# Performance work log

Measured on AMD Instinct MI355X. Metric: run time of the kernel, lower is better.

## Reference

```python
import jax, jax.numpy as jnp
import numpy as np

HEADS = 8
DIM_HEAD = 64
TAU = 0.001        # SoftSort temperature
TEMP = 10.0        # GammaAggregator temperature (EspAttention default temperature=10)
SCALE = DIM_HEAD ** -0.5


def setup_inputs() -> dict:
    key = jax.random.key(0)
    k1, k2, k3, k4 = jax.random.split(key, 4)
    x = jax.random.normal(k1, (4, 128, 512), jnp.float32)
    w_qkv = jax.random.normal(k2, (1536, 512), jnp.float32) * 0.02
    w_out = jax.random.normal(k3, (512, 512), jnp.float32) * 0.02
    b_out = jax.random.normal(k4, (512,), jnp.float32) * 0.02
    return {"x": x, "w_qkv": w_qkv, "w_out": w_out, "b_out": b_out}


def _softsort_p2(scores, tau):
    # scores: [B,H,N,L] -> s: [B,H,L,N]
    s = jnp.swapaxes(scores, -1, -2)
    sorted_s = -jnp.sort(-s, axis=-1)                 # descending sort along N
    # pairwise diff: [B,H,L,N(sorted),N(orig)]
    d = s[..., None, :] - sorted_s[..., :, None]
    return jax.nn.softmax(-(d * d) / tau, axis=-1)    # P_hat [B,H,L,N,N]


def reference(x, w_qkv, w_out, b_out):
    B, N, D = x.shape
    qkv = x @ w_qkv.T                                  # [B,N,3*inner]
    q, k, v = jnp.split(qkv, 3, axis=-1)
    def to_heads(t):
        return jnp.swapaxes(t.reshape(B, N, HEADS, DIM_HEAD), 1, 2)  # [B,H,N,d]
    q, k, v = to_heads(q), to_heads(k), to_heads(v)

    X = q * SCALE
    Y = k * SCALE

    Pu = _softsort_p2(X, TAU)                          # [B,H,L,N,N]
    Pv = _softsort_p2(Y, TAU)                          # [B,H,L,N,N]
    # Gamma = Pu^T @ Pv over the sorted axis
    Gamma = jnp.einsum('bhlki,bhlkj->bhlij', Pu, Pv)   # [B,H,L,N,N]

    # cdist(X, Y, p=2): [B,H,N,N]
    sq = (jnp.sum(X * X, -1)[..., :, None]
          + jnp.sum(Y * Y, -1)[..., None, :]
          - 2.0 * jnp.einsum('bhnd,bhmd->bhnm', X, Y))
    cost = jnp.sqrt(jnp.maximum(sq, 0.0))

    # swds_l = sum_ij cost_ij * Gamma_lij
    swds = jnp.einsum('bhij,bhlij->bhl', cost, Gamma)  # [B,H,L]
    min_s = jnp.min(swds, axis=-1, keepdims=True)
    e = jnp.exp(-TEMP * (swds - min_s))
    weights = e / jnp.sum(e, axis=-1, keepdims=True)   # [B,H,L]

    attn = jnp.einsum('bhl,bhlij->bhij', weights, Gamma)  # [B,H,N,N]

    out = jnp.einsum('bhij,bhjd->bhid', attn, v)       # [B,H,N,d]
    out = jnp.swapaxes(out, 1, 2).reshape(B, N, HEADS * DIM_HEAD)
    out = out @ w_out.T + b_out                        # to_out (dropout=0)
    return out, attn
```

## Files before the change

kernel.cpp:

```cpp
#include <hip/hip_runtime.h>
#include <math.h>

typedef _Float16 f16x8 __attribute__((ext_vector_type(8)));
typedef _Float16 f16x4 __attribute__((ext_vector_type(4)));
typedef float f32x4 __attribute__((ext_vector_type(4)));

#define NSEQ   128
#define DIMH   64
#define NHEAD  8
#define DMODEL 512
#define SCALE  0.125f
#define SPAD   136

#define OFF_X    0
#define OFF_Y    262144
#define OFF_V    524288
#define OFF_COST 786432
#define OFF_SWDS 1310720
#define OFF_W    1312768
#define OFF_OH   1314816
#define OFF_XT   1576960
#define OFF_YT   1839104
#define OFF_ST   2101248
#define OFF_PART 3674112
#define END_PART 12062720

#define PF_SMEM  (NSEQ * SPAD * 2 + (768 + 8) * 4)
#define PH_SMEM  (2 * NSEQ * SPAD * 2 + (128 * 3 + 512 + 8) * 4)

__device__ __forceinline__ f16x8 cvt8(f32x4 a, f32x4 b) {
  f16x8 h;
  h[0] = (_Float16)a[0]; h[1] = (_Float16)a[1]; h[2] = (_Float16)a[2]; h[3] = (_Float16)a[3];
  h[4] = (_Float16)b[0]; h[5] = (_Float16)b[1]; h[6] = (_Float16)b[2]; h[7] = (_Float16)b[3];
  return h;
}

__global__ __launch_bounds__(256) void k_qkv_f(const float* __restrict__ x,
                                               const float* __restrict__ wq,
                                               float* __restrict__ ws) {
  __shared__ _Float16 Ah[64][72];
  __shared__ _Float16 Bh[64][72];
  const int r0 = blockIdx.x * 64, c0 = blockIdx.y * 64;
  const int t = threadIdx.x, w = t >> 6, lane = t & 63;
  const int srow = t >> 2, sk = (t & 3) << 4;
  f32x4 acc[4] = {};
  for (int kc = 0; kc < 512; kc += 64) {
    __syncthreads();
    {
      const float* ap = &x[(size_t)(r0 + srow) * 512 + kc + sk];
      const float* bp = &wq[(size_t)(c0 + srow) * 512 + kc + sk];
      f32x4 a0 = *(const f32x4*)&ap[0], a1 = *(const f32x4*)&ap[4];
      f32x4 a2 = *(const f32x4*)&ap[8], a3 = *(const f32x4*)&ap[12];
      f32x4 b0 = *(const f32x4*)&bp[0], b1 = *(const f32x4*)&bp[4];
      f32x4 b2 = *(const f32x4*)&bp[8], b3 = *(const f32x4*)&bp[12];
      *(f16x8*)&Ah[srow][sk]     = cvt8(a0, a1);
      *(f16x8*)&Ah[srow][sk + 8] = cvt8(a2, a3);
      *(f16x8*)&Bh[srow][sk]     = cvt8(b0, b1);
      *(f16x8*)&Bh[srow][sk + 8] = cvt8(b2, b3);
    }
    __syncthreads();
#pragma unroll
    for (int k0 = 0; k0 < 64; k0 += 32) {
      f16x8 a = *(const f16x8*)&Ah[(w << 4) + (lane & 15)][k0 + ((lane >> 4) << 3)];
#pragma unroll
      for (int fj = 0; fj < 4; ++fj) {
        f16x8 b = *(const f16x8*)&Bh[(fj << 4) + (lane & 15)][k0 + ((lane >> 4) << 3)];
        acc[fj] = __builtin_amdgcn_mfma_f32_16x16x32_f16(a, b, acc[fj], 0, 0, 0);
      }
    }
  }
  float* X = ws + OFF_X; float* Y = ws + OFF_Y; float* V = ws + OFF_V;
  float* XT = ws + OFF_XT; float* YT = ws + OFF_YT;
  const int rowb = r0 + (w << 4) + ((lane >> 4) << 2);
#pragma unroll
  for (int fj = 0; fj < 4; ++fj) {
    const int c = c0 + (fj << 4) + (lane & 15);
    const int which = c >> 9, cc = c & 511, h = cc >> 6, d = cc & 63;
#pragma unroll
    for (int r = 0; r < 4; ++r) {
      const int rr = rowb + r, bb = rr >> 7, n = rr & 127;
      const int bh = bb * NHEAD + h;
      float val = acc[fj][r];
      size_t dst = ((size_t)bh * NSEQ + n) * DIMH + d;
      size_t dstT = ((size_t)bh * DIMH + d) * NSEQ + n;
      if (which == 0)      { X[dst] = val * SCALE; XT[dstT] = val * SCALE; }
      else if (which == 1) { Y[dst] = val * SCALE; YT[dstT] = val * SCALE; }
      else                 V[dst] = val;
    }
  }
}

__global__ __launch_bounds__(256) void k_qkv(const float* __restrict__ x,
                                             const float* __restrict__ wqkv,
                                             float* __restrict__ ws, int wrT) {
  __shared__ float xs[64][65];
  __shared__ float wsm[64][65];
  const int r0 = blockIdx.x * 64;
  const int c0 = blockIdx.y * 64;
  const int t = threadIdx.x;
  const int tr = (t >> 4) << 2;
  const int tc = (t & 15) << 2;
  float acc[4][4] = {};
  for (int k0 = 0; k0 < 512; k0 += 64) {
    for (int idx = t; idx < 64 * 64; idx += 256) {
      int i = idx >> 6, j = idx & 63;
      xs[i][j]  = x[(size_t)(r0 + i) * 512 + k0 + j];
      wsm[i][j] = wqkv[(size_t)(c0 + i) * 512 + k0 + j];
    }
    __syncthreads();
    for (int kk = 0; kk < 64; ++kk) {
      float a[4], b[4];
#pragma unroll
      for (int u = 0; u < 4; ++u) { a[u] = xs[tr + u][kk]; b[u] = wsm[tc + u][kk]; }
#pragma unroll
      for (int u = 0; u < 4; ++u)
#pragma unroll
        for (int w = 0; w < 4; ++w) acc[u][w] += a[u] * b[w];
    }
    __syncthreads();
  }
  float* X = ws + OFF_X; float* Y = ws + OFF_Y; float* V = ws + OFF_V;
  float* XT = ws + OFF_XT; float* YT = ws + OFF_YT;
#pragma unroll
  for (int u = 0; u < 4; ++u) {
    int r = r0 + tr + u; int b = r >> 7, n = r & 127;
#pragma unroll
    for (int w = 0; w < 4; ++w) {
      int c = c0 + tc + w;
      float val = acc[u][w];
      int which = c >> 9;
      int cc = c & 511;
      int h = cc >> 6, d = cc & 63;
      int bh = b * NHEAD + h;
      size_t dst = ((size_t)bh * NSEQ + n) * DIMH + d;
      size_t dstT = ((size_t)bh * DIMH + d) * NSEQ + n;
      if (which == 0)      { X[dst] = val * SCALE; if (wrT) XT[dstT] = val * SCALE; }
      else if (which == 1) { Y[dst] = val * SCALE; if (wrT) YT[dstT] = val * SCALE; }
      else                 V[dst] = val;
    }
  }
}

__global__ __launch_bounds__(256) void k_cost(float* __restrict__ ws) {
  __shared__ float Ys[128 * 64];
  __shared__ float Xs[16 * 64];
  __shared__ float xx[16], yy[128];
  const int bh = blockIdx.x, g = blockIdx.y;
  const int t = threadIdx.x;
  const float* Xg = ws + OFF_X + (size_t)bh * NSEQ * DIMH + (size_t)g * 16 * DIMH;
  const float* Yg = ws + OFF_Y + (size_t)bh * NSEQ * DIMH;
  for (int c = t; c < 1024; c += 256) Xs[c] = Xg[c];
  for (int c = t; c < 8192; c += 256) Ys[c] = Yg[c];
  __syncthreads();
  if (t < 128) {
    float s = 0;
    const f32x4* y4 = (const f32x4*)&Ys[t * 64];
#pragma unroll
    for (int d = 0; d < 16; ++d) { f32x4 v = y4[d]; s += v[0]*v[0]+v[1]*v[1]+v[2]*v[2]+v[3]*v[3]; }
    yy[t] = s;
  } else if (t < 144) {
    int i = t - 128; float s = 0;
    const f32x4* x4 = (const f32x4*)&Xs[i * 64];
#pragma unroll
    for (int d = 0; d < 16; ++d) { f32x4 v = x4[d]; s += v[0]*v[0]+v[1]*v[1]+v[2]*v[2]+v[3]*v[3]; }
    xx[i] = s;
  }
  __syncthreads();
  const int i = t >> 4, j0 = (t & 15) << 3;
  f32x4 xr[16];
#pragma unroll
  for (int d = 0; d < 16; ++d) xr[d] = ((const f32x4*)&Xs[i * 64])[d];
  const float xxi = xx[i];
  float* C = ws + OFF_COST + (size_t)bh * NSEQ * NSEQ + (size_t)(g * 16 + i) * NSEQ + j0;
  f32x4 o0, o1;
#pragma unroll
  for (int jj = 0; jj < 8; ++jj) {
    const f32x4* y4 = (const f32x4*)&Ys[(j0 + jj) * 64];
    float dot = 0;
#pragma unroll
    for (int d = 0; d < 16; ++d) {
      f32x4 xv = xr[d], yv = y4[d];
      dot += xv[0]*yv[0] + xv[1]*yv[1] + xv[2]*yv[2] + xv[3]*yv[3];
    }
    float sq = xxi + yy[j0 + jj] - 2.f * dot;
    float cv = sqrtf(fmaxf(sq, 0.f));
    if (jj < 4) o0[jj] = cv; else o1[jj - 4] = cv;
  }
  *(f32x4*)&C[0] = o0;
  *(f32x4*)&C[4] = o1;
}

__global__ __launch_bounds__(256) void k_sortden(float* __restrict__ ws) {
  __shared__ float s_lds[128], ss_lds[128], den2[256];
  const int bid = blockIdx.x;
  const int t = threadIdx.x;
  const float* src = ws + ((bid & 1) ? OFF_YT : OFF_XT) + (size_t)(bid >> 1) * NSEQ;
  float* st = ws + OFF_ST + (size_t)bid * 384;
  if (t < 128) s_lds[t] = src[t];
  __syncthreads();
  if (t < 128) {
    const float v = s_lds[t];
    int rank = 0;
#pragma unroll 4
    for (int m = 0; m < NSEQ; m += 4) {
      f32x4 u = *(const f32x4*)&s_lds[m];
#pragma unroll
      for (int j = 0; j < 4; ++j)
        rank += (u[j] > v) || (u[j] == v && (m + j) < t);
    }
    ss_lds[rank] = v;
  }
  __syncthreads();
  {
    const int k = t & 127, half = t >> 7;
    const float sk = ss_lds[k];
    const float* sb = s_lds + (half << 6);
    float sum = 0.f;
#pragma unroll 4
    for (int m = 0; m < 64; m += 4) {
      f32x4 u = *(const f32x4*)&sb[m];
#pragma unroll
      for (int j = 0; j < 4; ++j) {
        float d = u[j] - sk;
        sum += __expf(-1000.f * d * d);
      }
    }
    den2[(half << 7) + k] = sum;
  }
  __syncthreads();
  if (t < 128) {
    st[t]       = s_lds[t];
    st[128 + t] = ss_lds[t];
    st[256 + t] = 1.f / (den2[t] + den2[128 + t]);
  }
}

__device__ __forceinline__ void gen_PT(const float* __restrict__ st,
                                       _Float16* __restrict__ PT, int t) {
  const int i = t >> 2, k0 = (t & 3) << 5;
  const float si = st[i];
  const float* ssp = st + 128 + k0;
  const float* ivp = st + 256 + k0;
#pragma unroll
  for (int kb = 0; kb < 32; kb += 8) {
    f32x4 sv0 = *(const f32x4*)&ssp[kb];
    f32x4 sv1 = *(const f32x4*)&ssp[kb + 4];
    f32x4 iv0 = *(const f32x4*)&ivp[kb];
    f32x4 iv1 = *(const f32x4*)&ivp[kb + 4];
    f16x8 pk;
#pragma unroll
    for (int j = 0; j < 4; ++j) {
      float d0 = si - sv0[j];
      float d1 = si - sv1[j];
      pk[j]     = (_Float16)(__expf(-1000.f * d0 * d0) * iv0[j]);
      pk[j + 4] = (_Float16)(__expf(-1000.f * d1 * d1) * iv1[j]);
    }
    *reinterpret_cast<f16x8*>(&PT[i * SPAD + k0 + kb]) = pk;
  }
}

__device__ __forceinline__ f16x8 gen_Afrag(float si, const float* __restrict__ ss,
                                           const float* __restrict__ iv, int k) {
  f32x4 s0 = *(const f32x4*)&ss[k], s1 = *(const f32x4*)&ss[k + 4];
  f32x4 i0 = *(const f32x4*)&iv[k], i1 = *(const f32x4*)&iv[k + 4];
  f16x8 a;
#pragma unroll
  for (int j = 0; j < 4; ++j) {
    float d0 = si - s0[j];
    float d1 = si - s1[j];
    a[j]     = (_Float16)(__expf(-1000.f * d0 * d0) * i0[j]);
    a[j + 4] = (_Float16)(__expf(-1000.f * d1 * d1) * i1[j]);
  }
  return a;
}

__device__ void build_PT(const float* __restrict__ col, _Float16* __restrict__ PT,
                         float* s_, float* ss_, float* inv_, float* den4, int t) {
  if (t < NSEQ) s_[t] = col[(size_t)t * DIMH];
  __syncthreads();
  if (t < NSEQ) {
    const float v = s_[t];
    int rank = 0;
#pragma unroll 4
    for (int m = 0; m < NSEQ; m += 4) {
      f32x4 u = *(const f32x4*)&s_[m];
#pragma unroll
      for (int j = 0; j < 4; ++j)
        rank += (u[j] > v) || (u[j] == v && (m + j) < t);
    }
    ss_[rank] = v;
  }
  __syncthreads();
  {
    const int k = t & 127, q = t >> 7;
    const float sk = ss_[k];
    const float* sb = s_ + (q << 5);
    float sum = 0.f;
#pragma unroll 4
    for (int m = 0; m < 32; m += 4) {
      f32x4 u = *(const f32x4*)&sb[m];
#pragma unroll
      for (int j = 0; j < 4; ++j) {
        float d = u[j] - sk;
        sum += __expf(-1000.f * d * d);
      }
    }
    den4[(q << 7) + k] = sum;
  }
  __syncthreads();
  if (t < NSEQ)
    inv_[t] = 1.f / (den4[t] + den4[128 + t] + den4[256 + t] + den4[384 + t]);
  __syncthreads();
  {
    const int i = t >> 2, k0 = (t & 3) << 5;
    const float si = s_[i];
#pragma unroll
    for (int kb = 0; kb < 32; kb += 8) {
      f32x4 sv0 = *(const f32x4*)&ss_[k0 + kb];
      f32x4 sv1 = *(const f32x4*)&ss_[k0 + kb + 4];
      f32x4 iv0 = *(const f32x4*)&inv_[k0 + kb];
      f32x4 iv1 = *(const f32x4*)&inv_[k0 + kb + 4];
      f16x8 pk;
#pragma unroll
      for (int j = 0; j < 4; ++j) {
        float d0 = si - sv0[j];
        float d1 = si - sv1[j];
        pk[j]     = (_Float16)(__expf(-1000.f * d0 * d0) * iv0[j]);
        pk[j + 4] = (_Float16)(__expf(-1000.f * d1 * d1) * iv1[j]);
      }
      *reinterpret_cast<f16x8*>(&PT[i * SPAD + k0 + kb]) = pk;
    }
  }
  __syncthreads();
}

__device__ __forceinline__ f16x8 fragPT(const _Float16* PT, int baserow, int k0, int lane) {
  return *reinterpret_cast<const f16x8*>(
      &PT[(baserow + (lane & 15)) * SPAD + k0 + ((lane >> 4) << 3)]);
}

__global__ __launch_bounds__(512, 4) void k_pf(float* __restrict__ ws) {
  extern __shared__ char smem[];
  _Float16* PvT = (_Float16*)smem;
  float* aux = (float*)(PvT + NSEQ * SPAD);
  float* red = aux + 768;
  const int blk = blockIdx.x, bh = blk >> 4, lc = blk & 15;
  const int t = threadIdx.x, w = t >> 6, lane = t & 63;
  const int r0 = w << 4;
  const int kq = (lane >> 4) << 3;
  const float* C = ws + OFF_COST + (size_t)bh * NSEQ * NSEQ;
  const int cr = r0 + ((lane >> 4) << 2), cc = lane & 15;
  f32x4 att[8];
#pragma unroll
  for (int b = 0; b < 8; ++b) att[b] = 0;
  float m_run = 3.0e38f, Z = 0.f;
  for (int q = 0; q < 4; ++q) {
    const int l = (lc << 2) + q;
    if (q) __syncthreads();
    const float* stg = ws + OFF_ST + (size_t)(bh * 64 + l) * 768;
    for (int i = t; i < 768; i += 512) aux[i] = stg[i];
    __syncthreads();
    gen_PT(aux + 384, PvT, t);
    __syncthreads();
    const float si = aux[r0 + (lane & 15)];
    const float* ssu = aux + 128;
    const float* ivu = aux + 256;
    f32x4 acc[8];
#pragma unroll
    for (int b = 0; b < 8; ++b) acc[b] = 0;
#pragma unroll
    for (int kc = 0; kc < 4; ++kc) {
      const int k0 = kc << 5;
      f16x8 a = gen_Afrag(si, ssu, ivu, k0 + kq);
#pragma unroll
      for (int fj = 0; fj < 8; ++fj) {
        f16x8 b = fragPT(PvT, fj << 4, k0, lane);
        acc[fj] = __builtin_amdgcn_mfma_f32_16x16x32_f16(a, b, acc[fj], 0, 0, 0);
      }
    }
    float part = 0.f;
#pragma unroll
    for (int fj = 0; fj < 8; ++fj)
#pragma unroll
      for (int r = 0; r < 4; ++r)
        part += acc[fj][r] * C[(cr + r) * NSEQ + (fj << 4) + cc];
#pragma unroll
    for (int off = 32; off >= 1; off >>= 1) part += __shfl_xor(part, off);
    if (lane == 0) red[w] = part;
    __syncthreads();
    float swds = ((red[0] + red[1]) + (red[2] + red[3]))
               + ((red[4] + red[5]) + (red[6] + red[7]));
    if (swds < m_run) {
      float sc = __expf(-10.f * (m_run - swds));
      Z = Z * sc + 1.f;
#pragma unroll
      for (int b = 0; b < 8; ++b) att[b] = att[b] * sc + acc[b];
      m_run = swds;
    } else {
      float e = __expf(-10.f * (swds - m_run));
      Z += e;
#pragma unroll
      for (int b = 0; b < 8; ++b) att[b] += e * acc[b];
    }
  }
  float* P = ws + OFF_PART + (size_t)blk * (NSEQ * NSEQ);
#pragma unroll
  for (int fj = 0; fj < 8; ++fj)
#pragma unroll
    for (int r = 0; r < 4; ++r)
      P[(cr + r) * NSEQ + (fj << 4) + cc] = att[fj][r];
  if (t == 0) {
    ws[OFF_SWDS + blk * 2]     = m_run;
    ws[OFF_SWDS + blk * 2 + 1] = Z;
  }
}

__global__ __launch_bounds__(512, 4) void k_phase1_fb(float* __restrict__ ws) {
  extern __shared__ char smem[];
  _Float16* PuT = (_Float16*)smem;
  _Float16* PvT = PuT + NSEQ * SPAD;
  float* s_   = (float*)(PvT + NSEQ * SPAD);
  float* ss_  = s_ + 128;
  float* inv_ = ss_ + 128;
  float* den4 = inv_ + 128;
  float* red  = den4 + 512;
  const int bhl = blockIdx.x, bh = bhl >> 6, l = bhl & 63;
  const int t = threadIdx.x, w = t >> 6, lane = t & 63;
  build_PT(ws + OFF_X + (size_t)bh * NSEQ * DIMH + l, PuT, s_, ss_, inv_, den4, t);
  build_PT(ws + OFF_Y + (size_t)bh * NSEQ * DIMH + l, PvT, s_, ss_, inv_, den4, t);
  f32x4 acc[8];
#pragma unroll
  for (int b = 0; b < 8; ++b) acc[b] = 0;
  const int r0 = w << 4;
#pragma unroll
  for (int kc = 0; kc < 4; ++kc) {
    const int k0 = kc << 5;
    f16x8 a0 = fragPT(PuT, r0, k0, lane);
#pragma unroll
    for (int fj = 0; fj < 8; ++fj) {
      f16x8 b = fragPT(PvT, fj << 4, k0, lane);
      acc[fj] = __builtin_amdgcn_mfma_f32_16x16x32_f16(a0, b, acc[fj], 0, 0, 0);
    }
  }
  const float* C = ws + OFF_COST + (size_t)bh * NSEQ * NSEQ;
  const int cr = r0 + ((lane >> 4) << 2), cc = lane & 15;
  float part = 0.f;
#pragma unroll
  for (int fj = 0; fj < 8; ++fj)
#pragma unroll
    for (int r = 0; r < 4; ++r)
      part += acc[fj][r] * C[(cr + r) * NSEQ + (fj << 4) + cc];
#pragma unroll
  for (int off = 32; off >= 1; off >>= 1) part += __shfl_xor(part, off);
  if (lane == 0) red[w] = part;
  __syncthreads();
  if (t == 0) {
    float s = 0;
#pragma unroll
    for (int i = 0; i < 8; ++i) s += red[i];
    ws[OFF_SWDS + bhl] = s;
  }
}

__global__ void k_weights(float* __restrict__ ws) {
  const int bh = blockIdx.x;
  const int l = threadIdx.x;
  float v = ws[OFF_SWDS + bh * 64 + l];
  float mn = v;
#pragma unroll
  for (int off = 32; off >= 1; off >>= 1) mn = fminf(mn, __shfl_xor(mn, off));
  float e = __expf(-10.f * (v - mn));
  float sum = e;
#pragma unroll
  for (int off = 32; off >= 1; off >>= 1) sum += __shfl_xor(sum, off);
  ws[OFF_W + bh * 64 + l] = e / sum;
}

__global__ __launch_bounds__(512, 4) void k_phase2_fb(float* __restrict__ ws, float* __restrict__ attn) {
  extern __shared__ char smem[];
  _Float16* PuT = (_Float16*)smem;
  _Float16* PvT = PuT + NSEQ * SPAD;
  float* s_   = (float*)(PvT + NSEQ * SPAD);
  float* ss_  = s_ + 128;
  float* inv_ = ss_ + 128;
  float* den4 = inv_ + 128;
  const int blk = blockIdx.x, bh = blk >> 4, lc = blk & 15;
  const int t = threadIdx.x, w = t >> 6, lane = t & 63;
  const int r0 = w << 4;
  f32x4 att[8];
#pragma unroll
  for (int b = 0; b < 8; ++b) att[b] = 0;
  for (int q = 0; q < 4; ++q) {
    const int l = (lc << 2) + q;
    const float wl = ws[OFF_W + bh * 64 + l];
    build_PT(ws + OFF_X + (size_t)bh * NSEQ * DIMH + l, PuT, s_, ss_, inv_, den4, t);
    build_PT(ws + OFF_Y + (size_t)bh * NSEQ * DIMH + l, PvT, s_, ss_, inv_, den4, t);
    f32x4 acc[8];
#pragma unroll
    for (int b = 0; b < 8; ++b) acc[b] = 0;
#pragma unroll
    for (int kc = 0; kc < 4; ++kc) {
      const int k0 = kc << 5;
      f16x8 a0 = fragPT(PuT, r0, k0, lane);
#pragma unroll
      for (int fj = 0; fj < 8; ++fj) {
        f16x8 b = fragPT(PvT, fj << 4, k0, lane);
        acc[fj] = __builtin_amdgcn_mfma_f32_16x16x32_f16(a0, b, acc[fj], 0, 0, 0);
      }
    }
#pragma unroll
    for (int b = 0; b < 8; ++b) att[b] += wl * acc[b];
  }
  float* A = attn + (size_t)bh * NSEQ * NSEQ;
  const int cr = r0 + ((lane >> 4) << 2), cc = lane & 15;
#pragma unroll
  for (int fj = 0; fj < 8; ++fj)
#pragma unroll
    for (int r = 0; r < 4; ++r)
      atomicAdd(&A[(cr + r) * NSEQ + (fj << 4) + cc], att[fj][r]);
}

__global__ __launch_bounds__(256) void k_avr(float* __restrict__ ws, float* __restrict__ attn) {
  __shared__ float Vs[128 * 64];
  __shared__ float As[16 * 128];
  __shared__ float F[16];
  __shared__ float Zinv_s;
  const int bh = blockIdx.x, g = blockIdx.y;
  const int t = threadIdx.x;
  for (int c = t; c < 8192; c += 256) Vs[c] = ws[OFF_V + (size_t)bh * 8192 + c];
  if (t == 0) {
    float mb[16], zb[16], m = 3.0e38f;
#pragma unroll
    for (int p = 0; p < 16; ++p) {
      mb[p] = ws[OFF_SWDS + (bh * 16 + p) * 2];
      zb[p] = ws[OFF_SWDS + (bh * 16 + p) * 2 + 1];
      m = fminf(m, mb[p]);
    }
    float Zt = 0.f;
#pragma unroll
    for (int p = 0; p < 16; ++p) {
      float f = __expf(-10.f * (mb[p] - m));
      F[p] = f;
      Zt += f * zb[p];
    }
    Zinv_s = 1.f / Zt;
  }
  __syncthreads();
  const float zi = Zinv_s;
  for (int c = t; c < 2048; c += 256) {
    float s = 0.f;
#pragma unroll
    for (int p = 0; p < 16; ++p)
      s += F[p] * ws[OFF_PART + ((size_t)(bh * 16 + p)) * 16384 + (size_t)g * 2048 + c];
    s *= zi;
    As[c] = s;
    attn[(size_t)bh * 16384 + (size_t)g * 2048 + c] = s;
  }
  __syncthreads();
  const int i = t >> 4, dq = t & 15;
  f32x4 acc = {};
  const float* arow = &As[i * 128];
  for (int j = 0; j < 128; ++j) {
    float a = arow[j];
    f32x4 v = ((const f32x4*)&Vs[j * 64])[dq];
    acc += a * v;
  }
  const int b = bh >> 3, h = bh & 7, n = g * 16 + i;
  const size_t obase = ((size_t)(b * NSEQ + n)) * DMODEL + h * DIMH + (dq << 2);
  _Float16* oh16 = (_Float16*)(ws + OFF_XT + 131072) + obase;
  f16x4 hh;
  hh[0] = (_Float16)acc[0]; hh[1] = (_Float16)acc[1];
  hh[2] = (_Float16)acc[2]; hh[3] = (_Float16)acc[3];
  *(f16x4*)oh16 = hh;
}

__global__ __launch_bounds__(256) void k_av(const float* __restrict__ attn, float* __restrict__ ws) {
  __shared__ float Vs[128 * 64];
  __shared__ float As[16 * 128];
  const int bh = blockIdx.x, g = blockIdx.y;
  const int t = threadIdx.x;
  const float* Ag = attn + (size_t)bh * 16384 + (size_t)g * 16 * 128;
  const float* Vg = ws + OFF_V + (size_t)bh * 8192;
  for (int c = t; c < 2048; c += 256) As[c] = Ag[c];
  for (int c = t; c < 8192; c += 256) Vs[c] = Vg[c];
  __syncthreads();
  const int i = t >> 4, dq = t & 15;
  f32x4 acc = {};
  const float* arow = &As[i * 128];
  for (int j = 0; j < 128; ++j) {
    float a = arow[j];
    f32x4 v = ((const f32x4*)&Vs[j * 64])[dq];
    acc += a * v;
  }
  const int b = bh >> 3, h = bh & 7, n = g * 16 + i;
  const size_t obase = ((size_t)(b * NSEQ + n)) * DMODEL + h * DIMH + (dq << 2);
  float* o = ws + OFF_OH + obase;
  *(f32x4*)o = acc;
}

__global__ __launch_bounds__(256) void k_out_f(const float* __restrict__ ws_c,
                                               const float* __restrict__ wout,
                                               const float* __restrict__ bout,
                                               float* __restrict__ out) {
  __shared__ _Float16 Ah[64][72];
  __shared__ _Float16 Bh[64][72];
  const _Float16* ah = (const _Float16*)(ws_c + OFF_XT + 131072);
  const int r0 = blockIdx.x * 64, c0 = blockIdx.y * 64;
  const int t = threadIdx.x, w = t >> 6, lane = t & 63;
  const int srow = t >> 2, sk = (t & 3) << 4;
  f32x4 acc[4] = {};
  for (int kc = 0; kc < 512; kc += 64) {
    __syncthreads();
    {
      *(f16x8*)&Ah[srow][sk]     = *(const f16x8*)&ah[(size_t)(r0 + srow) * 512 + kc + sk];
      *(f16x8*)&Ah[srow][sk + 8] = *(const f16x8*)&ah[(size_t)(r0 + srow) * 512 + kc + sk + 8];
      const float* bp = &wout[(size_t)(c0 + srow) * 512 + kc + sk];
      f32x4 b0 = *(const f32x4*)&bp[0], b1 = *(const f32x4*)&bp[4];
      f32x4 b2 = *(const f32x4*)&bp[8], b3 = *(const f32x4*)&bp[12];
      *(f16x8*)&Bh[srow][sk]     = cvt8(b0, b1);
      *(f16x8*)&Bh[srow][sk + 8] = cvt8(b2, b3);
    }
    __syncthreads();
#pragma unroll
    for (int k0 = 0; k0 < 64; k0 += 32) {
      f16x8 a = *(const f16x8*)&Ah[(w << 4) + (lane & 15)][k0 + ((lane >> 4) << 3)];
#pragma unroll
      for (int fj = 0; fj < 4; ++fj) {
        f16x8 b = *(const f16x8*)&Bh[(fj << 4) + (lane & 15)][k0 + ((lane >> 4) << 3)];
        acc[fj] = __builtin_amdgcn_mfma_f32_16x16x32_f16(a, b, acc[fj], 0, 0, 0);
      }
    }
  }
  const int rowb = r0 + (w << 4) + ((lane >> 4) << 2);
#pragma unroll
  for (int fj = 0; fj < 4; ++fj) {
    const int c = c0 + (fj << 4) + (lane & 15);
    const float bb = bout[c];
#pragma unroll
    for (int r = 0; r < 4; ++r)
      out[(size_t)(rowb + r) * 512 + c] = acc[fj][r] + bb;
  }
}

__global__ __launch_bounds__(256) void k_out(const float* __restrict__ oh,
                                             const float* __restrict__ wout,
                                             const float* __restrict__ bout,
                                             float* __restrict__ out) {
  __shared__ float as_[64][65];
  __shared__ float bs_[64][65];
  const int r0 = blockIdx.x * 64, c0 = blockIdx.y * 64;
  const int t = threadIdx.x;
  const int tr = (t >> 4) << 2, tc = (t & 15) << 2;
  float acc[4][4] = {};
  for (int k0 = 0; k0 < 512; k0 += 64) {
    for (int idx = t; idx < 64 * 64; idx += 256) {
      int i = idx >> 6, j = idx & 63;
      as_[i][j] = oh[(size_t)(r0 + i) * 512 + k0 + j];
      bs_[i][j] = wout[(size_t)(c0 + i) * 512 + k0 + j];
    }
    __syncthreads();
    for (int kk = 0; kk < 64; ++kk) {
      float a[4], b[4];
#pragma unroll
      for (int u = 0; u < 4; ++u) { a[u] = as_[tr + u][kk]; b[u] = bs_[tc + u][kk]; }
#pragma unroll
      for (int u = 0; u < 4; ++u)
#pragma unroll
        for (int w = 0; w < 4; ++w) acc[u][w] += a[u] * b[w];
    }
    __syncthreads();
  }
#pragma unroll
  for (int u = 0; u < 4; ++u)
#pragma unroll
    for (int w = 0; w < 4; ++w)
      out[(size_t)(r0 + tr + u) * 512 + c0 + tc + w] = acc[u][w] + bout[c0 + tc + w];
}

extern "C" void kernel_launch(void* const* d_in, const int* in_sizes, int n_in,
                              void* d_out, int out_size, void* d_ws, size_t ws_size,
                              hipStream_t stream) {
  (void)in_sizes; (void)n_in; (void)out_size;
  const float* x    = (const float*)d_in[0];
  const float* wqkv = (const float*)d_in[1];
  const float* wout = (const float*)d_in[2];
  const float* bout = (const float*)d_in[3];
  float* out  = (float*)d_out;
  float* attn = out + 262144;
  float* ws   = (float*)d_ws;

  const bool fast = ws_size >= (size_t)END_PART * 4;

  if (fast) {
    k_qkv_f<<<dim3(8, 24), 256, 0, stream>>>(x, wqkv, ws);
    k_cost<<<dim3(32, 8), 256, 0, stream>>>(ws);
    k_sortden<<<4096, 256, 0, stream>>>(ws);
    k_pf<<<512, 512, PF_SMEM, stream>>>(ws);
    k_avr<<<dim3(32, 8), 256, 0, stream>>>(ws, attn);
    k_out_f<<<dim3(8, 8), 256, 0, stream>>>(ws, wout, bout, out);
  } else {
    k_qkv<<<dim3(8, 24), 256, 0, stream>>>(x, wqkv, ws, 0);
    k_cost<<<dim3(32, 8), 256, 0, stream>>>(ws);
    k_phase1_fb<<<2048, 512, PH_SMEM, stream>>>(ws);
    k_weights<<<32, 64, 0, stream>>>(ws);
    hipMemsetAsync(attn, 0, 524288 * sizeof(float), stream);
    k_phase2_fb<<<512, 512, PH_SMEM, stream>>>(ws, attn);
    k_av<<<dim3(32, 8), 256, 0, stream>>>(attn, ws);
    k_out<<<dim3(8, 8), 256, 0, stream>>>(ws + OFF_OH, wout, bout, out);
  }
}
```

Baseline: 134.7 us.

## Split k_pf across twice as many blocks and prefetch next slice stats

k_pf now processes two L-slices per block instead of four, doubling the grid to 1024 blocks and raising the launch-bounds occupancy hint to 8. Stats for the second slice are loaded during the first iteration, and gen_PT's thread-to-row mapping is changed. k_avr reduces 32 partials using warp shuffles instead of a single serial thread. When workspace is too small for fp32 partials, they are stored as fp16. The cost is twice the partial-attention traffic in k_avr, plus reduced precision on the fp16 path.

```diff
diff --git a/kernel.cpp b/kernel.cpp
--- a/kernel.cpp
+++ b/kernel.cpp
@@ -237,7 +237,7 @@
 
 __device__ __forceinline__ void gen_PT(const float* __restrict__ st,
                                        _Float16* __restrict__ PT, int t) {
-  const int i = t >> 2, k0 = (t & 3) << 5;
+  const int i = t & 127, k0 = (t >> 7) << 5;
   const float si = st[i];
   const float* ssp = st + 128 + k0;
   const float* ivp = st + 256 + k0;
@@ -339,12 +339,13 @@
       &PT[(baserow + (lane & 15)) * SPAD + k0 + ((lane >> 4) << 3)]);
 }
 
-__global__ __launch_bounds__(512, 4) void k_pf(float* __restrict__ ws) {
+template <bool HALFP>
+__global__ __launch_bounds__(512, 8) void k_pf(float* __restrict__ ws) {
   extern __shared__ char smem[];
   _Float16* PvT = (_Float16*)smem;
   float* aux = (float*)(PvT + NSEQ * SPAD);
   float* red = aux + 768;
-  const int blk = blockIdx.x, bh = blk >> 4, lc = blk & 15;
+  const int blk = blockIdx.x, bh = blk >> 5, lc = blk & 31;
   const int t = threadIdx.x, w = t >> 6, lane = t & 63;
   const int r0 = w << 4;
   const int kq = (lane >> 4) << 3;
@@ -354,11 +355,12 @@
 #pragma unroll
   for (int b = 0; b < 8; ++b) att[b] = 0;
   float m_run = 3.0e38f, Z = 0.f;
-  for (int q = 0; q < 4; ++q) {
-    const int l = (lc << 2) + q;
-    if (q) __syncthreads();
-    const float* stg = ws + OFF_ST + (size_t)(bh * 64 + l) * 768;
-    for (int i = t; i < 768; i += 512) aux[i] = stg[i];
+  {
+    const float* stg = ws + OFF_ST + (size_t)(bh * 64 + lc * 2) * 768;
+    aux[t] = stg[t];
+    if (t < 256) aux[t + 512] = stg[t + 512];
+  }
+  for (int q = 0; q < 2; ++q) {
     __syncthreads();
     gen_PT(aux + 384, PvT, t);
     __syncthreads();
@@ -402,13 +404,27 @@
 #pragma unroll
       for (int b = 0; b < 8; ++b) att[b] += e * acc[b];
     }
-  }
-  float* P = ws + OFF_PART + (size_t)blk * (NSEQ * NSEQ);
-#pragma unroll
-  for (int fj = 0; fj < 8; ++fj)
-#pragma unroll
-    for (int r = 0; r < 4; ++r)
-      P[(cr + r) * NSEQ + (fj << 4) + cc] = att[fj][r];
+    if (q == 0) {
+      const float* stg = ws + OFF_ST + (size_t)(bh * 64 + lc * 2 + 1) * 768;
+      aux[t] = stg[t];
+      if (t < 256) aux[t + 512] = stg[t + 512];
+    }
+  }
+  if (HALFP) {
+    _Float16* P = (_Float16*)(ws + OFF_PART) + (size_t)blk * (NSEQ * NSEQ);
+#pragma unroll
+    for (int fj = 0; fj < 8; ++fj)
+#pragma unroll
+      for (int r = 0; r < 4; ++r)
+        P[(cr + r) * NSEQ + (fj << 4) + cc] = (_Float16)att[fj][r];
+  } else {
+    float* P = ws + OFF_PART + (size_t)blk * (NSEQ * NSEQ);
+#pragma unroll
+    for (int fj = 0; fj < 8; ++fj)
+#pragma unroll
+      for (int r = 0; r < 4; ++r)
+        P[(cr + r) * NSEQ + (fj << 4) + cc] = att[fj][r];
+  }
   if (t == 0) {
     ws[OFF_SWDS + blk * 2]     = m_run;
     ws[OFF_SWDS + blk * 2 + 1] = Z;
@@ -520,38 +536,44 @@
       atomicAdd(&A[(cr + r) * NSEQ + (fj << 4) + cc], att[fj][r]);
 }
 
+template <bool HALFP>
 __global__ __launch_bounds__(256) void k_avr(float* __restrict__ ws, float* __restrict__ attn) {
   __shared__ float Vs[128 * 64];
   __shared__ float As[16 * 128];
-  __shared__ float F[16];
+  __shared__ float F[32];
   __shared__ float Zinv_s;
   const int bh = blockIdx.x, g = blockIdx.y;
   const int t = threadIdx.x;
   for (int c = t; c < 8192; c += 256) Vs[c] = ws[OFF_V + (size_t)bh * 8192 + c];
-  if (t == 0) {
-    float mb[16], zb[16], m = 3.0e38f;
-#pragma unroll
-    for (int p = 0; p < 16; ++p) {
-      mb[p] = ws[OFF_SWDS + (bh * 16 + p) * 2];
-      zb[p] = ws[OFF_SWDS + (bh * 16 + p) * 2 + 1];
-      m = fminf(m, mb[p]);
-    }
-    float Zt = 0.f;
-#pragma unroll
-    for (int p = 0; p < 16; ++p) {
-      float f = __expf(-10.f * (mb[p] - m));
-      F[p] = f;
-      Zt += f * zb[p];
-    }
-    Zinv_s = 1.f / Zt;
+  if (t < 64) {
+    const int p = t & 31;
+    float mb = ws[OFF_SWDS + (bh * 32 + p) * 2];
+    float zb = ws[OFF_SWDS + (bh * 32 + p) * 2 + 1];
+    float m = mb;
+#pragma unroll
+    for (int off = 16; off >= 1; off >>= 1) m = fminf(m, __shfl_xor(m, off));
+    float f = __expf(-10.f * (mb - m));
+    float fz = f * zb;
+    float Zt = fz;
+#pragma unroll
+    for (int off = 16; off >= 1; off >>= 1) Zt += __shfl_xor(fz, off), fz = Zt;
+    if (t < 32) F[t] = f;
+    if (t == 0) Zinv_s = 1.f / Zt;
   }
   __syncthreads();
   const float zi = Zinv_s;
   for (int c = t; c < 2048; c += 256) {
     float s = 0.f;
-#pragma unroll
-    for (int p = 0; p < 16; ++p)
-      s += F[p] * ws[OFF_PART + ((size_t)(bh * 16 + p)) * 16384 + (size_t)g * 2048 + c];
+    if (HALFP) {
+      const _Float16* P = (const _Float16*)(ws + OFF_PART);
+#pragma unroll
+      for (int p = 0; p < 32; ++p)
+        s += F[p] * (float)P[((size_t)(bh * 32 + p)) * 16384 + (size_t)g * 2048 + c];
+    } else {
+#pragma unroll
+      for (int p = 0; p < 32; ++p)
+        s += F[p] * ws[OFF_PART + ((size_t)(bh * 32 + p)) * 16384 + (size_t)g * 2048 + c];
+    }
     s *= zi;
     As[c] = s;
     attn[(size_t)bh * 16384 + (size_t)g * 2048 + c] = s;
@@ -689,14 +711,20 @@
   float* attn = out + 262144;
   float* ws   = (float*)d_ws;
 
-  const bool fast = ws_size >= (size_t)END_PART * 4;
-
-  if (fast) {
+  const size_t need_f16 = (size_t)END_PART * 4;
+  const size_t need_f32 = ((size_t)OFF_PART + 1024ull * 16384) * 4;
+
+  if (ws_size >= need_f16) {
     k_qkv_f<<<dim3(8, 24), 256, 0, stream>>>(x, wqkv, ws);
     k_cost<<<dim3(32, 8), 256, 0, stream>>>(ws);
     k_sortden<<<4096, 256, 0, stream>>>(ws);
-    k_pf<<<512, 512, PF_SMEM, stream>>>(ws);
-    k_avr<<<dim3(32, 8), 256, 0, stream>>>(ws, attn);
+    if (ws_size >= need_f32) {
+      k_pf<false><<<1024, 512, PF_SMEM, stream>>>(ws);
+      k_avr<false><<<dim3(32, 8), 256, 0, stream>>>(ws, attn);
+    } else {
+      k_pf<true><<<1024, 512, PF_SMEM, stream>>>(ws);
+      k_avr<true><<<dim3(32, 8), 256, 0, stream>>>(ws, attn);
+    }
     k_out_f<<<dim3(8, 8), 256, 0, stream>>>(ws, wout, bout, out);
   } else {
     k_qkv<<<dim3(8, 24), 256, 0, stream>>>(x, wqkv, ws, 0);
```

Result: slower. 217.7 us (+61.5%).

## Prefetch all four sort states and overlap PvT generation with cost reduction

Applied to the files above, without the earlier changes.

In k_pf the four per-l sort states are now loaded into shared memory once at the start, and the next PvT tile is generated right after the MFMA loop, overlapping with the cost-weighted reduction. This removes per-iteration global loads and one barrier per iteration. gen_PT's thread-to-row mapping changes to i = t & 127, which alters the shared-memory store pattern. In k_avr, the serial single-thread min/normalizer computation is replaced by a 16-lane shuffle reduction. Shared memory use grows by about 9 KB per block, which may lower occupancy.

```diff
diff --git a/kernel.cpp b/kernel.cpp
--- a/kernel.cpp
+++ b/kernel.cpp
@@ -25,7 +25,7 @@
 #define OFF_PART 3674112
 #define END_PART 12062720
 
-#define PF_SMEM  (NSEQ * SPAD * 2 + (768 + 8) * 4)
+#define PF_SMEM  (NSEQ * SPAD * 2 + (4 * 768 + 8) * 4)
 #define PH_SMEM  (2 * NSEQ * SPAD * 2 + (128 * 3 + 512 + 8) * 4)
 
 __device__ __forceinline__ f16x8 cvt8(f32x4 a, f32x4 b) {
@@ -237,7 +237,7 @@
 
 __device__ __forceinline__ void gen_PT(const float* __restrict__ st,
                                        _Float16* __restrict__ PT, int t) {
-  const int i = t >> 2, k0 = (t & 3) << 5;
+  const int i = t & 127, k0 = (t >> 7) << 5;
   const float si = st[i];
   const float* ssp = st + 128 + k0;
   const float* ivp = st + 256 + k0;
@@ -343,7 +343,7 @@
   extern __shared__ char smem[];
   _Float16* PvT = (_Float16*)smem;
   float* aux = (float*)(PvT + NSEQ * SPAD);
-  float* red = aux + 768;
+  float* red = aux + 4 * 768;
   const int blk = blockIdx.x, bh = blk >> 4, lc = blk & 15;
   const int t = threadIdx.x, w = t >> 6, lane = t & 63;
   const int r0 = w << 4;
@@ -354,17 +354,18 @@
 #pragma unroll
   for (int b = 0; b < 8; ++b) att[b] = 0;
   float m_run = 3.0e38f, Z = 0.f;
+  {
+    const float* stg = ws + OFF_ST + (size_t)(bh * 64 + lc * 4) * 768;
+    for (int i = t; i < 3072; i += 512) aux[i] = stg[i];
+  }
+  __syncthreads();
+  gen_PT(aux + 384, PvT, t);
+  __syncthreads();
   for (int q = 0; q < 4; ++q) {
-    const int l = (lc << 2) + q;
-    if (q) __syncthreads();
-    const float* stg = ws + OFF_ST + (size_t)(bh * 64 + l) * 768;
-    for (int i = t; i < 768; i += 512) aux[i] = stg[i];
-    __syncthreads();
-    gen_PT(aux + 384, PvT, t);
-    __syncthreads();
-    const float si = aux[r0 + (lane & 15)];
-    const float* ssu = aux + 128;
-    const float* ivu = aux + 256;
+    const float* a_st = aux + q * 768;
+    const float si = a_st[r0 + (lane & 15)];
+    const float* ssu = a_st + 128;
+    const float* ivu = a_st + 256;
     f32x4 acc[8];
 #pragma unroll
     for (int b = 0; b < 8; ++b) acc[b] = 0;
@@ -378,12 +379,14 @@
         acc[fj] = __builtin_amdgcn_mfma_f32_16x16x32_f16(a, b, acc[fj], 0, 0, 0);
       }
     }
+    __syncthreads();
     float part = 0.f;
 #pragma unroll
     for (int fj = 0; fj < 8; ++fj)
 #pragma unroll
       for (int r = 0; r < 4; ++r)
         part += acc[fj][r] * C[(cr + r) * NSEQ + (fj << 4) + cc];
+    if (q < 3) gen_PT(aux + (q + 1) * 768 + 384, PvT, t);
 #pragma unroll
     for (int off = 32; off >= 1; off >>= 1) part += __shfl_xor(part, off);
     if (lane == 0) red[w] = part;
@@ -528,22 +531,19 @@
   const int bh = blockIdx.x, g = blockIdx.y;
   const int t = threadIdx.x;
   for (int c = t; c < 8192; c += 256) Vs[c] = ws[OFF_V + (size_t)bh * 8192 + c];
-  if (t == 0) {
-    float mb[16], zb[16], m = 3.0e38f;
-#pragma unroll
-    for (int p = 0; p < 16; ++p) {
-      mb[p] = ws[OFF_SWDS + (bh * 16 + p) * 2];
-      zb[p] = ws[OFF_SWDS + (bh * 16 + p) * 2 + 1];
-      m = fminf(m, mb[p]);
-    }
-    float Zt = 0.f;
-#pragma unroll
-    for (int p = 0; p < 16; ++p) {
-      float f = __expf(-10.f * (mb[p] - m));
-      F[p] = f;
-      Zt += f * zb[p];
-    }
-    Zinv_s = 1.f / Zt;
+  if (t < 32) {
+    const int p = t & 15;
+    float mb = ws[OFF_SWDS + (bh * 16 + p) * 2];
+    float zb = ws[OFF_SWDS + (bh * 16 + p) * 2 + 1];
+    float m = mb;
+#pragma unroll
+    for (int off = 8; off >= 1; off >>= 1) m = fminf(m, __shfl_xor(m, off));
+    float f = __expf(-10.f * (mb - m));
+    float s = f * zb;
+#pragma unroll
+    for (int off = 8; off >= 1; off >>= 1) s += __shfl_xor(s, off);
+    if (t < 16) F[t] = f;
+    if (t == 0) Zinv_s = 1.f / s;
   }
   __syncthreads();
   const float zi = Zinv_s;
```

New measurement: 139.8 us. 1.04x slower.
